# Optimization experiments

Measured on AMD Instinct MI355X. Metric: run time of the kernel, lower is better.

The kernel has to match this reference:

```python
import jax, jax.numpy as jnp
import numpy as np

STRIDE = 1
PADDING = 1
DILATION = 1


def setup_inputs() -> dict:
    key = jax.random.key(0)
    k1, k2, k3 = jax.random.split(key, 3)
    b_i, b_j, c, h, w = 32, 1, 128, 32, 32
    oc, kh, kw = 128, 3, 3
    x = jax.random.normal(k1, (b_i, b_j, c, h, w), dtype=jnp.float32)
    weight = jax.random.normal(k2, (b_i, oc, c, kh, kw), dtype=jnp.float32) * 0.05
    bias = jax.random.normal(k3, (b_i, b_j, oc), dtype=jnp.float32) * 0.05
    return {"x": x, "weight": weight, "bias": bias}


def reference(x, weight, bias):
    # x: [b_i, b_j, c, h, w]; weight: [b_i, oc, c, kh, kw]; bias: [b_i, b_j, oc]
    b_i, b_j, c, h, w = x.shape
    oc, kh, kw = weight.shape[1], weight.shape[3], weight.shape[4]
    # fold per-sample dim into channels, run one grouped conv with groups=b_i
    xr = jnp.transpose(x, (1, 0, 2, 3, 4)).reshape(b_j, b_i * c, h, w)
    wr = weight.reshape(b_i * oc, c, kh, kw)
    out = jax.lax.conv_general_dilated(
        xr, wr,
        window_strides=(STRIDE, STRIDE),
        padding=[(PADDING, PADDING), (PADDING, PADDING)],
        rhs_dilation=(DILATION, DILATION),
        dimension_numbers=("NCHW", "OIHW", "NCHW"),
        feature_group_count=b_i,
    )  # [b_j, b_i*oc, H, W]
    H, W = out.shape[-2], out.shape[-1]
    out = out.reshape(b_j, b_i, oc, H, W).transpose(1, 0, 2, 3, 4)  # [b_i, b_j, oc, H, W]
    out = out + bias[:, :, :, None, None]
    return out
```

## Files before the change

### kernel.cpp

```cpp
#include <hip/hip_runtime.h>

typedef unsigned short u16;
typedef unsigned int u32;
typedef __attribute__((ext_vector_type(2))) unsigned int u32x2;
typedef __attribute__((ext_vector_type(8))) short bf16x8;
typedef __attribute__((ext_vector_type(4))) float f32x4;

#define CIN 128
#define OC 128
#define NP 1024
#define KTOT 1152
#define NSTEP 18
#define BK 64
#define TILE_U16 8192
#define SAMP_U16 (NSTEP * TILE_U16)

typedef const u32 __attribute__((address_space(1)))* gptr_t;
typedef u32 __attribute__((address_space(3)))* lptr_t;

__device__ __forceinline__ u16 f2bf(float f) {
  unsigned b = __builtin_bit_cast(unsigned, f);
  b += 0x7fffu + ((b >> 16) & 1u);
  return (u16)(b >> 16);
}

__global__ void wcvt_kernel(const float* __restrict__ w, u16* __restrict__ wbf2) {
  __shared__ u16 lds[KTOT];
  const int blk = blockIdx.x;
  const int t = threadIdx.x;
  const int i = blk >> 7, row = blk & 127;
  const float* src = w + (size_t)blk * KTOT;
#pragma unroll
  for (int e = 0; e < 9; ++e) {
    int idx = t + 128 * e;
    lds[idx] = f2bf(src[idx]);
  }
  __syncthreads();
  u16* dst = wbf2 + (size_t)i * SAMP_U16;
  const int rsw = row & 7;
#pragma unroll
  for (int e = 0; e < 9; ++e) {
    const int o = t + 128 * e;
    const int s = o >> 6;
    const int slotk = (o >> 3) & 7;
    const int ee = o & 7;
    dst[s * TILE_U16 + (row * 8 + (slotk ^ rsw)) * 8 + ee] = lds[t * 9 + e];
  }
}

__global__ __launch_bounds__(256, 1) void conv_mfma(
    const float* __restrict__ x,
    const u16* __restrict__ wbf2,
    const float* __restrict__ bias,
    float* __restrict__ out) {
  __shared__ u16 Xs[6 * 34 * 128];
  __shared__ u16 Asw[3][TILE_U16];

  const int wg = (int)blockIdx.x;
  const int swz = (wg & 7) * 32 + (wg >> 3);
  const int i  = swz >> 3;
  const int pt = swz & 7;
  const int p0 = pt * 128;
  const int tid = (int)threadIdx.x;
  const int lane = tid & 63;
  const int wid = tid >> 6;
  const int wm = wid >> 1;
  const int wn = wid & 1;
  const int lcol = lane & 15;
  const int lhi  = lane >> 4;

  const float* xi = x + (size_t)i * CIN * NP;
  const u16*   wt = wbf2 + (size_t)i * SAMP_U16;

#define STAGE(step, buf) do {                                          \
    const char* _tb = (const char*)(wt + (step) * TILE_U16);           \
    _Pragma("unroll")                                                  \
    for (int _j = 0; _j < 4; ++_j) {                                   \
      const int _off = wid * 4096 + _j * 1024;                         \
      __builtin_amdgcn_global_load_lds(                                \
          (gptr_t)(_tb + _off + lane * 16),                            \
          (lptr_t)((char*)&Asw[buf][0] + _off), 16, 0, 0);             \
    }                                                                  \
  } while (0)

  STAGE(0, 0);
  STAGE(1, 1);

  {
    const int xx = tid & 31;
    const int cg = tid >> 5;
    const int col = xx + 1;
    const int csw = col & 7;
#pragma unroll
    for (int r = 0; r < 6; ++r) {
      const int yr = 4 * pt - 1 + r;
      float v[16];
      if ((unsigned)yr < 32u) {
        const float* src = xi + (size_t)(cg * 16) * NP + yr * 32 + xx;
#pragma unroll
        for (int j = 0; j < 16; ++j) v[j] = src[(size_t)j * NP];
      } else {
#pragma unroll
        for (int j = 0; j < 16; ++j) v[j] = 0.f;
      }
      u32 pk[8];
#pragma unroll
      for (int m = 0; m < 8; ++m)
        pk[m] = (u32)f2bf(v[2 * m]) | ((u32)f2bf(v[2 * m + 1]) << 16);
#pragma unroll
      for (int q = 0; q < 4; ++q) {
        const int cslot = cg * 2 + (q >> 1);
        const int idx = ((r * 34 + col) * 16 + (cslot ^ csw)) * 8 + (q & 1) * 4;
        *(u32x2*)(&Xs[idx]) = (u32x2){pk[2 * q], pk[2 * q + 1]};
      }
    }
    if (tid < 192) {
      const int r = tid / 32;
      const int hc = ((tid >> 4) & 1) ? 33 : 0;
      const int s = tid & 15;
      const int idx = ((r * 34 + hc) * 16 + (s ^ (hc & 7))) * 8;
      *(bf16x8*)(&Xs[idx]) = (bf16x8){0, 0, 0, 0, 0, 0, 0, 0};
    }
  }

  f32x4 acc[4][4];
#pragma unroll
  for (int mi = 0; mi < 4; ++mi)
#pragma unroll
    for (int ni = 0; ni < 4; ++ni)
      acc[mi][ni] = (f32x4){0.f, 0.f, 0.f, 0.f};

  __syncthreads();

#pragma unroll
  for (int step = 0; step < NSTEP; ++step) {
    const int buf = step % 3;
    const int rs = step >> 1;
    const int r3 = rs / 3;
    const int dy = r3 - 1;
    const int dx = (rs - r3 * 3) - 1;
    const int c0s = (step & 1) * 8;

    if (step + 2 < NSTEP) STAGE(step + 2, (step + 2) % 3);

    __builtin_amdgcn_s_setprio(1);
#pragma unroll
    for (int kkk = 0; kkk < 2; ++kkk) {
      bf16x8 af[4], bfr[4];
#pragma unroll
      for (int mi = 0; mi < 4; ++mi) {
        const int row = wm * 64 + mi * 16 + lcol;
        const int slot = (kkk * 4 + lhi) ^ (row & 7);
        af[mi] = *(const bf16x8*)(&Asw[buf][row * BK + slot * 8]);
      }
#pragma unroll
      for (int ni = 0; ni < 4; ++ni) {
        const int srow = wn * 2 + (ni >> 1) + 1 + dy;
        const int col  = (ni & 1) * 16 + lcol + 1 + dx;
        const int cslot = c0s + kkk * 4 + lhi;
        const int idx = ((srow * 34 + col) * 16 + (cslot ^ (col & 7))) * 8;
        bfr[ni] = *(const bf16x8*)(&Xs[idx]);
      }
#pragma unroll
      for (int mi = 0; mi < 4; ++mi)
#pragma unroll
        for (int ni = 0; ni < 4; ++ni)
          acc[mi][ni] = __builtin_amdgcn_mfma_f32_16x16x32_bf16(
              af[mi], bfr[ni], acc[mi][ni], 0, 0, 0);
    }
    __builtin_amdgcn_s_setprio(0);

    if (step + 2 < NSTEP) {
      asm volatile("s_waitcnt vmcnt(4)" ::: "memory");
    } else if (step + 1 < NSTEP) {
      asm volatile("s_waitcnt vmcnt(0)" ::: "memory");
    }
    if (step + 1 < NSTEP) {
      __builtin_amdgcn_s_barrier();
      __builtin_amdgcn_sched_barrier(0);
    }
  }

  const int row0 = lhi * 4;
#pragma unroll
  for (int mi = 0; mi < 4; ++mi) {
    const int oc = wm * 64 + mi * 16 + row0;
#pragma unroll
    for (int jj = 0; jj < 4; ++jj) {
      const float bv = bias[i * OC + oc + jj];
      float* orow = out + ((size_t)i * OC + oc + jj) * NP;
#pragma unroll
      for (int ni = 0; ni < 4; ++ni) {
        const int pg = p0 + wn * 64 + ni * 16 + lcol;
        orow[pg] = acc[mi][ni][jj] + bv;
      }
    }
  }
#undef STAGE
}

extern "C" void kernel_launch(void* const* d_in, const int* in_sizes, int n_in,
                              void* d_out, int out_size, void* d_ws, size_t ws_size,
                              hipStream_t stream) {
  const float* x    = (const float*)d_in[0];
  const float* w    = (const float*)d_in[1];
  const float* bias = (const float*)d_in[2];
  float* out = (float*)d_out;
  u16* wbf2 = (u16*)d_ws;

  wcvt_kernel<<<dim3(32 * OC), dim3(128), 0, stream>>>(w, wbf2);
  conv_mfma<<<dim3(256), dim3(256), 0, stream>>>(x, wbf2, bias, out);
}
```

Measured before the change: 33.90 us.

## Double waves per block to 8 with smaller per-wave tiles and 4-buffer pipeline

Launches 512 threads per block, splitting the 128x128 output tile across 8 waves (2x4) each computing 64x32, with 4 LDS weight buffers and waits/barriers moved before compute. Each wave preloads both k-halves of fragments before issuing MFMAs. The aim is more latency hiding per CU since the grid is only 256 blocks, at the cost of more redundant LDS A-fragment reads and an extra barrier per step.

```diff
diff --git a/kernel.cpp b/kernel.cpp
--- a/kernel.cpp
+++ b/kernel.cpp
@@ -48,13 +48,13 @@
   }
 }
 
-__global__ __launch_bounds__(256, 1) void conv_mfma(
+__global__ __launch_bounds__(512, 1) void conv_mfma(
     const float* __restrict__ x,
     const u16* __restrict__ wbf2,
     const float* __restrict__ bias,
     float* __restrict__ out) {
   __shared__ u16 Xs[6 * 34 * 128];
-  __shared__ u16 Asw[3][TILE_U16];
+  __shared__ u16 Asw[4][TILE_U16];
 
   const int wg = (int)blockIdx.x;
   const int swz = (wg & 7) * 32 + (wg >> 3);
@@ -64,35 +64,38 @@
   const int tid = (int)threadIdx.x;
   const int lane = tid & 63;
   const int wid = tid >> 6;
-  const int wm = wid >> 1;
-  const int wn = wid & 1;
+  const int wm = wid >> 2;
+  const int wn = wid & 3;
   const int lcol = lane & 15;
   const int lhi  = lane >> 4;
 
   const float* xi = x + (size_t)i * CIN * NP;
   const u16*   wt = wbf2 + (size_t)i * SAMP_U16;
 
-#define STAGE(step, buf) do {                                          \
+#define STAGE(step) do {                                               \
     const char* _tb = (const char*)(wt + (step) * TILE_U16);           \
+    char* _lb = (char*)&Asw[(step) & 3][0];                            \
     _Pragma("unroll")                                                  \
-    for (int _j = 0; _j < 4; ++_j) {                                   \
-      const int _off = wid * 4096 + _j * 1024;                         \
+    for (int _j = 0; _j < 2; ++_j) {                                   \
+      const int _off = wid * 2048 + _j * 1024;                         \
       __builtin_amdgcn_global_load_lds(                                \
           (gptr_t)(_tb + _off + lane * 16),                            \
-          (lptr_t)((char*)&Asw[buf][0] + _off), 16, 0, 0);             \
+          (lptr_t)(_lb + _off), 16, 0, 0);                             \
     }                                                                  \
   } while (0)
 
-  STAGE(0, 0);
-  STAGE(1, 1);
+  STAGE(0);
+  STAGE(1);
 
   {
     const int xx = tid & 31;
-    const int cg = tid >> 5;
+    const int cg = (tid >> 5) & 7;
+    const int rh = tid >> 8;
     const int col = xx + 1;
     const int csw = col & 7;
 #pragma unroll
-    for (int r = 0; r < 6; ++r) {
+    for (int rr = 0; rr < 3; ++rr) {
+      const int r = rh * 3 + rr;
       const int yr = 4 * pt - 1 + r;
       float v[16];
       if ((unsigned)yr < 32u) {
@@ -123,62 +126,65 @@
     }
   }
 
-  f32x4 acc[4][4];
+  f32x4 acc[4][2];
 #pragma unroll
   for (int mi = 0; mi < 4; ++mi)
 #pragma unroll
-    for (int ni = 0; ni < 4; ++ni)
+    for (int ni = 0; ni < 2; ++ni)
       acc[mi][ni] = (f32x4){0.f, 0.f, 0.f, 0.f};
 
   __syncthreads();
 
 #pragma unroll
   for (int step = 0; step < NSTEP; ++step) {
-    const int buf = step % 3;
+    const int buf = step & 3;
     const int rs = step >> 1;
     const int r3 = rs / 3;
     const int dy = r3 - 1;
     const int dx = (rs - r3 * 3) - 1;
     const int c0s = (step & 1) * 8;
 
-    if (step + 2 < NSTEP) STAGE(step + 2, (step + 2) % 3);
-
-    __builtin_amdgcn_s_setprio(1);
+    if (step + 2 < NSTEP) STAGE(step + 2);
+
+    if (step + 2 < NSTEP) {
+      asm volatile("s_waitcnt vmcnt(4)" ::: "memory");
+    } else if (step + 1 < NSTEP) {
+      asm volatile("s_waitcnt vmcnt(2)" ::: "memory");
+    } else {
+      asm volatile("s_waitcnt vmcnt(0)" ::: "memory");
+    }
+    __builtin_amdgcn_s_barrier();
+    __builtin_amdgcn_sched_barrier(0);
+
+    bf16x8 af[2][4], bfr[2][2];
 #pragma unroll
     for (int kkk = 0; kkk < 2; ++kkk) {
-      bf16x8 af[4], bfr[4];
 #pragma unroll
       for (int mi = 0; mi < 4; ++mi) {
         const int row = wm * 64 + mi * 16 + lcol;
         const int slot = (kkk * 4 + lhi) ^ (row & 7);
-        af[mi] = *(const bf16x8*)(&Asw[buf][row * BK + slot * 8]);
-      }
-#pragma unroll
-      for (int ni = 0; ni < 4; ++ni) {
-        const int srow = wn * 2 + (ni >> 1) + 1 + dy;
-        const int col  = (ni & 1) * 16 + lcol + 1 + dx;
+        af[kkk][mi] = *(const bf16x8*)(&Asw[buf][row * BK + slot * 8]);
+      }
+#pragma unroll
+      for (int ni = 0; ni < 2; ++ni) {
+        const int srow = wn + 1 + dy;
+        const int col  = ni * 16 + lcol + 1 + dx;
         const int cslot = c0s + kkk * 4 + lhi;
         const int idx = ((srow * 34 + col) * 16 + (cslot ^ (col & 7))) * 8;
-        bfr[ni] = *(const bf16x8*)(&Xs[idx]);
-      }
+        bfr[kkk][ni] = *(const bf16x8*)(&Xs[idx]);
+      }
+    }
+    __builtin_amdgcn_s_setprio(1);
+#pragma unroll
+    for (int kkk = 0; kkk < 2; ++kkk)
 #pragma unroll
       for (int mi = 0; mi < 4; ++mi)
 #pragma unroll
-        for (int ni = 0; ni < 4; ++ni)
+        for (int ni = 0; ni < 2; ++ni)
           acc[mi][ni] = __builtin_amdgcn_mfma_f32_16x16x32_bf16(
-              af[mi], bfr[ni], acc[mi][ni], 0, 0, 0);
-    }
+              af[kkk][mi], bfr[kkk][ni], acc[mi][ni], 0, 0, 0);
     __builtin_amdgcn_s_setprio(0);
-
-    if (step + 2 < NSTEP) {
-      asm volatile("s_waitcnt vmcnt(4)" ::: "memory");
-    } else if (step + 1 < NSTEP) {
-      asm volatile("s_waitcnt vmcnt(0)" ::: "memory");
-    }
-    if (step + 1 < NSTEP) {
-      __builtin_amdgcn_s_barrier();
-      __builtin_amdgcn_sched_barrier(0);
-    }
+    __builtin_amdgcn_s_barrier();
   }
 
   const int row0 = lhi * 4;
@@ -190,8 +196,8 @@
       const float bv = bias[i * OC + oc + jj];
       float* orow = out + ((size_t)i * OC + oc + jj) * NP;
 #pragma unroll
-      for (int ni = 0; ni < 4; ++ni) {
-        const int pg = p0 + wn * 64 + ni * 16 + lcol;
+      for (int ni = 0; ni < 2; ++ni) {
+        const int pg = p0 + wn * 32 + ni * 16 + lcol;
         orow[pg] = acc[mi][ni][jj] + bv;
       }
     }
@@ -209,5 +215,5 @@
   u16* wbf2 = (u16*)d_ws;
 
   wcvt_kernel<<<dim3(32 * OC), dim3(128), 0, stream>>>(w, wbf2);
-  conv_mfma<<<dim3(256), dim3(256), 0, stream>>>(x, wbf2, bias, out);
-}
+  conv_mfma<<<dim3(256), dim3(512), 0, stream>>>(x, wbf2, bias, out);
+}
```

After: 30.64 us. 1.11x faster.
